# Optimization experiments

Hardware: AMD Instinct MI355X
Metric: run time of the kernel (lower is better)

The kernel has to match this reference:

```python
import jax, jax.numpy as jnp
import numpy as np

B, S, D = 2, 2048, 2048
H, KV, HD = 16, 4, 128          # n_heads, n_kv_heads, head_dim = d_model // n_heads
R = H // KV                      # n_rep (GQA group size)
THETA = 500000.0


def _rotate_half(x):
    x1, x2 = jnp.split(x, 2, axis=-1)
    return jnp.concatenate([-x2, x1], axis=-1)


def _rope_cos_sin(position_ids):
    # inv_freq over even dims, outer with positions, duplicated (LLaMA-style)
    inv_freq = 1.0 / (THETA ** (jnp.arange(0, HD, 2, dtype=jnp.float32) / HD))
    freqs = position_ids.astype(jnp.float32)[..., None] * inv_freq  # (B, S, HD/2)
    emb = jnp.concatenate([freqs, freqs], axis=-1)                  # (B, S, HD)
    return jnp.cos(emb)[:, None], jnp.sin(emb)[:, None]             # (B, 1, S, HD)


def setup_inputs() -> dict:
    key = jax.random.key(0)
    ks = jax.random.split(key, 5)
    x = jax.random.normal(ks[0], (B, S, D), dtype=jnp.float32)
    wq = jax.random.normal(ks[1], (D, H * HD), dtype=jnp.float32) * (D ** -0.5)
    wk = jax.random.normal(ks[2], (D, KV * HD), dtype=jnp.float32) * (D ** -0.5)
    wv = jax.random.normal(ks[3], (D, KV * HD), dtype=jnp.float32) * (D ** -0.5)
    wo = jax.random.normal(ks[4], (H * HD, D), dtype=jnp.float32) * (D ** -0.5)
    causal = jnp.tril(jnp.ones((S, S), dtype=bool))
    attn_mask = jnp.where(causal, 0.0, -1e9).astype(jnp.float32)[None, None]  # (1,1,S,S)
    position_ids = jnp.tile(jnp.arange(S, dtype=jnp.int32)[None, :], (B, 1))
    return {"x": x, "wq": wq, "wk": wk, "wv": wv, "wo": wo,
            "attn_mask": attn_mask, "position_ids": position_ids}


def reference(x, wq, wk, wv, wo, attn_mask, position_ids):
    b, s, _ = x.shape
    # projections (bias-free Linear) + head split, (B, heads, S, HD)
    q = (x @ wq).reshape(b, s, H, HD).transpose(0, 2, 1, 3)
    k = (x @ wk).reshape(b, s, KV, HD).transpose(0, 2, 1, 3)
    v = (x @ wv).reshape(b, s, KV, HD).transpose(0, 2, 1, 3)
    cos, sin = _rope_cos_sin(position_ids)
    q = q * cos + _rotate_half(q) * sin
    k = k * cos + _rotate_half(k) * sin
    # GQA: group q heads (B, KV, R, S, HD); equivalent to repeat_interleave on K/V
    qg = q.reshape(b, KV, R, s, HD)
    scores = jnp.einsum('bgrsd,bgtd->bgrst', qg.astype(jnp.float32),
                        k.astype(jnp.float32)) / np.float32(np.sqrt(HD))
    scores = scores + attn_mask[:, :, None]          # (1,1,1,S,S) broadcast
    p = jax.nn.softmax(scores, axis=-1).astype(x.dtype)
    out = jnp.einsum('bgrst,bgtd->bgrsd', p, v)      # (B, KV, R, S, HD)
    out = out.reshape(b, H, s, HD).transpose(0, 2, 1, 3).reshape(b, s, H * HD)
    return out @ wo
```

## Files before the change

kernel.cpp:

```cpp
#include <hip/hip_runtime.h>
#include <hip/hip_bf16.h>
#include <math.h>

#define Bsz 2
#define Sq  2048
#define Dm  2048
#define Hn  16
#define KVn 4
#define HDn 128

typedef __attribute__((ext_vector_type(8))) short bf16x8;
typedef __attribute__((ext_vector_type(4))) float f32x4;

__device__ __forceinline__ short f2b(float f) {
    __hip_bfloat16 h = __float2bfloat16(f);
    return *reinterpret_cast<short*>(&h);
}
__device__ __forceinline__ float b2f(short s) {
    __hip_bfloat16 h = *reinterpret_cast<__hip_bfloat16*>(&s);
    return __bfloat162float(h);
}

__global__ __launch_bounds__(256) void f2b_kernel(
    const float* __restrict__ X, short* __restrict__ Y, int n4)
{
    int i = blockIdx.x * 256 + threadIdx.x;
    if (i >= n4) return;
    float4 v = ((const float4*)X)[i];
    short4 o;
    o.x = f2b(v.x); o.y = f2b(v.y); o.z = f2b(v.z); o.w = f2b(v.w);
    ((short4*)Y)[i] = o;
}

__global__ __launch_bounds__(256) void wconv_all_kernel(
    const float* __restrict__ wq, const float* __restrict__ wk,
    const float* __restrict__ wv, const float* __restrict__ wo,
    short* __restrict__ wqkvT, short* __restrict__ woT)
{
    __shared__ float t[32][33];
    const int n0 = blockIdx.x * 32;
    const int k0 = blockIdx.y * 32;
    const int tx = threadIdx.x, ty = threadIdx.y;

    const float* W; int Nsec, nloc; short* dst;
    if (n0 < 2048)      { W = wq; Nsec = 2048; nloc = n0;        dst = wqkvT + (size_t)n0 * Dm; }
    else if (n0 < 2560) { W = wk; Nsec = 512;  nloc = n0 - 2048; dst = wqkvT + (size_t)n0 * Dm; }
    else if (n0 < 3072) { W = wv; Nsec = 512;  nloc = n0 - 2560; dst = wqkvT + (size_t)n0 * Dm; }
    else                { W = wo; Nsec = 2048; nloc = n0 - 3072; dst = woT + (size_t)(n0 - 3072) * Dm; }

#pragma unroll
    for (int r = 0; r < 4; ++r) {
        const int row = ty + 8 * r;
        t[row][tx] = W[(size_t)(k0 + row) * Nsec + nloc + tx];
    }
    __syncthreads();
#pragma unroll
    for (int r = 0; r < 4; ++r) {
        const int row = ty + 8 * r;
        dst[(size_t)row * Dm + k0 + tx] = f2b(t[tx][row]);
    }
}

template <typename OT>
__global__ __launch_bounds__(256) void gemm_bt_kernel(
    const short* __restrict__ A, const short* __restrict__ Bt,
    OT* __restrict__ C, int M, int N, int K)
{
    __shared__ __align__(16) short As[128 * 64];
    __shared__ __align__(16) short Bs[128 * 64];

    const int tid  = threadIdx.x;
    const int w    = tid >> 6;
    const int lane = tid & 63;
    const int m16  = lane & 15;
    const int g4   = lane >> 4;
    const int wm   = w >> 1, wn = w & 1;

    const int row0 = blockIdx.y * 128;
    const int col0 = blockIdx.x * 128;

    const short* Ab = A  + (size_t)row0 * K;
    const short* Bb = Bt + (size_t)col0 * K;

    const int trow = tid >> 3;
    const int soct = (tid & 7) ^ (trow & 7);

    f32x4 acc[4][4];
#pragma unroll
    for (int i = 0; i < 4; ++i)
#pragma unroll
        for (int j = 0; j < 4; ++j) acc[i][j] = (f32x4){0.f, 0.f, 0.f, 0.f};

    for (int k0 = 0; k0 < K; k0 += 64) {
#pragma unroll
        for (int r = 0; r < 4; ++r) {
            const short* gp = Ab + (size_t)(r * 32 + trow) * K + k0 + soct * 8;
            short* lp = &As[(size_t)(r * 256 + w * 64) * 8];
            __builtin_amdgcn_global_load_lds(
                (const __attribute__((address_space(1))) void*)gp,
                (__attribute__((address_space(3))) void*)lp, 16, 0, 0);
        }
#pragma unroll
        for (int r = 0; r < 4; ++r) {
            const short* gp = Bb + (size_t)(r * 32 + trow) * K + k0 + soct * 8;
            short* lp = &Bs[(size_t)(r * 256 + w * 64) * 8];
            __builtin_amdgcn_global_load_lds(
                (const __attribute__((address_space(1))) void*)gp,
                (__attribute__((address_space(3))) void*)lp, 16, 0, 0);
        }
        __syncthreads();

#pragma unroll
        for (int kc = 0; kc < 2; ++kc) {
            bf16x8 a[4], b[4];
            const int swz = (kc * 4 + g4) ^ (m16 & 7);
#pragma unroll
            for (int s = 0; s < 4; ++s) {
                const int rowA = wm * 64 + s * 16 + m16;
                a[s] = *(const bf16x8*)&As[rowA * 64 + swz * 8];
                const int rowB = wn * 64 + s * 16 + m16;
                b[s] = *(const bf16x8*)&Bs[rowB * 64 + swz * 8];
            }
#pragma unroll
            for (int i = 0; i < 4; ++i)
#pragma unroll
                for (int j = 0; j < 4; ++j)
                    acc[i][j] = __builtin_amdgcn_mfma_f32_16x16x32_bf16(
                        a[i], b[j], acc[i][j], 0, 0, 0);
        }
        __syncthreads();
    }

#pragma unroll
    for (int i = 0; i < 4; ++i) {
        const int mbase = row0 + wm * 64 + i * 16 + g4 * 4;
#pragma unroll
        for (int j = 0; j < 4; ++j) {
            const int n = col0 + wn * 64 + j * 16 + m16;
#pragma unroll
            for (int r = 0; r < 4; ++r) {
                if constexpr (sizeof(OT) == 2)
                    C[(size_t)(mbase + r) * N + n] = f2b(acc[i][j][r]);
                else
                    C[(size_t)(mbase + r) * N + n] = acc[i][j][r];
            }
        }
    }
}

__global__ __launch_bounds__(256) void rope_all_kernel(
    const short* __restrict__ C3b, short* __restrict__ Qb, short* __restrict__ Kb,
    const int* __restrict__ pos_ids, float qscale, int total)
{
    int idx = blockIdx.x * blockDim.x + threadIdx.x;
    if (idx >= total) return;
    const int i = idx & 63;
    int rest = idx >> 6;
    const int s = rest % Sq;
    const int b = rest / Sq;

    const int pos = pos_ids[b * Sq + s];
    const float e   = -(float)(2 * i) * (1.0f / (float)HDn);
    const float inv = exp2f(e * 18.931568569324174f);
    const float f   = (float)pos * inv;
    float sn, c;
    sincosf(f, &sn, &c);

    const short* src = C3b + ((size_t)(b * Sq + s)) * 3072;

#pragma unroll
    for (int h = 0; h < Hn; ++h) {
        const float x1 = b2f(src[h * HDn + i]);
        const float x2 = b2f(src[h * HDn + i + 64]);
        const size_t dst = (((size_t)b * Hn + h) * Sq + s) * HDn;
        Qb[dst + i]      = f2b((x1 * c - x2 * sn) * qscale);
        Qb[dst + i + 64] = f2b((x2 * c + x1 * sn) * qscale);
    }
#pragma unroll
    for (int h = 0; h < KVn; ++h) {
        const float x1 = b2f(src[2048 + h * HDn + i]);
        const float x2 = b2f(src[2048 + h * HDn + i + 64]);
        const size_t dst = (((size_t)b * KVn + h) * Sq + s) * HDn;
        Kb[dst + i]      = f2b(x1 * c - x2 * sn);
        Kb[dst + i + 64] = f2b(x2 * c + x1 * sn);
    }
}

__global__ __launch_bounds__(256) void vconv_kernel(
    const short* __restrict__ C3b, short* __restrict__ Vt)
{
    __shared__ short t[32][34];
    const int bk = blockIdx.z;
    const int b  = bk >> 2, kv = bk & 3;
    const int s0 = blockIdx.x * 32;
    const int d0 = blockIdx.y * 32;
    const int tx = threadIdx.x, ty = threadIdx.y;

#pragma unroll
    for (int r = 0; r < 4; ++r) {
        const int row = ty + 8 * r;
        t[row][tx] = C3b[((size_t)(b * Sq + s0 + row)) * 3072 + 2560 + kv * HDn + d0 + tx];
    }
    __syncthreads();
#pragma unroll
    for (int r = 0; r < 4; ++r) {
        const int row = ty + 8 * r;
        Vt[((size_t)bk * HDn + d0 + row) * Sq + s0 + tx] = t[tx][row];
    }
}

__global__ __launch_bounds__(256, 2) void fattn_kernel(
    const short* __restrict__ Qb, const short* __restrict__ Kb,
    const short* __restrict__ Vtb, short* __restrict__ AOb)
{
    __shared__ __align__(16) short Ks[2][64 * 128];
    __shared__ __align__(16) short Vs[2][128 * 64];

    const int tid  = threadIdx.x;
    const int w    = tid >> 6;
    const int lane = tid & 63;
    const int m16  = lane & 15;
    const int g4   = lane >> 4;

    const int i    = blockIdx.x;
    const int half = i >> 8;
    const int k4   = i & 15;
    const int p    = half ? k4 : 15 - k4;
    const int h    = (i >> 4) & 15;
    const int b    = i >> 8;
    const int kv   = h >> 2;

    const int htA = 31 - p, htB = p;
    const int nch = htA + 1;
    const int qA  = htA * 64 + w * 16;
    const int qB  = htB * 64 + w * 16;

    bf16x8 qfA[4], qfB[4];
    {
        const short* qpA = Qb + (((size_t)b * Hn + h) * Sq + qA + m16) * HDn + g4 * 8;
        const short* qpB = Qb + (((size_t)b * Hn + h) * Sq + qB + m16) * HDn + g4 * 8;
#pragma unroll
        for (int c = 0; c < 4; ++c) {
            qfA[c] = *(const bf16x8*)(qpA + c * 32);
            qfB[c] = *(const bf16x8*)(qpB + c * 32);
        }
    }

    const short* kbase = Kb  + ((size_t)b * KVn + kv) * Sq * HDn;
    const short* vbase = Vtb + ((size_t)b * KVn + kv) * (size_t)HDn * Sq;

    const short* gpK[4];
    const short* gpV[4];
#pragma unroll
    for (int r = 0; r < 4; ++r) {
        const int ci = r * 256 + tid;
        const int R  = ci >> 4, o = ci & 15;
        const int hf = (R >> 5) & 1, Rl = R & 31;
        const int phys = hf * 32 + ((Rl >> 2) & 3) * 8 + ((Rl >> 4) & 1) * 4 + (Rl & 3);
        gpK[r] = kbase + (size_t)phys * HDn + (o ^ (R & 7)) * 8;
        const int d = ci >> 3, ov = ci & 7;
        gpV[r] = vbase + (size_t)d * Sq + (ov ^ (d & 7)) * 8;
    }

    auto stage = [&](int ktE, int buf) {
#pragma unroll
        for (int r = 0; r < 4; ++r) {
            const short* gp = gpK[r] + (size_t)ktE * HDn;
            short* lp = &Ks[buf][(size_t)(r * 256 + w * 64) * 8];
            __builtin_amdgcn_global_load_lds(
                (const __attribute__((address_space(1))) void*)gp,
                (__attribute__((address_space(3))) void*)lp, 16, 0, 0);
        }
#pragma unroll
        for (int r = 0; r < 4; ++r) {
            const short* gp = gpV[r] + ktE;
            short* lp = &Vs[buf][(size_t)(r * 256 + w * 64) * 8];
            __builtin_amdgcn_global_load_lds(
                (const __attribute__((address_space(1))) void*)gp,
                (__attribute__((address_space(3))) void*)lp, 16, 0, 0);
        }
    };

    f32x4 OtA[8], OtB[8];
#pragma unroll
    for (int t = 0; t < 8; ++t) {
        OtA[t] = (f32x4){0.f, 0.f, 0.f, 0.f};
        OtB[t] = (f32x4){0.f, 0.f, 0.f, 0.f};
    }
    float mA = -1e30f, lA = 0.f, mB = -1e30f, lB = 0.f;

    stage(0, 0);
    int gpar = 0;

    for (int ch = 0; ch <= p; ++ch) {
        const int cur = gpar & 1; gpar ^= 1;
        const int kt  = ch << 6;

        __syncthreads();
        stage((ch + 1) << 6, cur ^ 1);

        const bool dgB = (ch == p);
        const short* KsC = Ks[cur];
        const short* VsC = Vs[cur];

        f32x4 sc0[4], sc1[4];
        __builtin_amdgcn_s_setprio(1);
#pragma unroll
        for (int f = 0; f < 4; ++f) {
            f32x4 a0 = (f32x4){0.f, 0.f, 0.f, 0.f};
            f32x4 a1 = (f32x4){0.f, 0.f, 0.f, 0.f};
            const int krow = f * 16 + m16;
#pragma unroll
            for (int c = 0; c < 4; ++c) {
                bf16x8 kf = *(const bf16x8*)&KsC[krow * 128 + (((c * 4 + g4) ^ (m16 & 7)) * 8)];
                a0 = __builtin_amdgcn_mfma_f32_16x16x32_bf16(kf, qfA[c], a0, 0, 0, 0);
                a1 = __builtin_amdgcn_mfma_f32_16x16x32_bf16(kf, qfB[c], a1, 0, 0, 0);
            }
            sc0[f] = a0; sc1[f] = a1;
        }
        __builtin_amdgcn_s_setprio(0);

        if (dgB) {
            const int qg = qB + m16;
#pragma unroll
            for (int f = 0; f < 4; ++f)
#pragma unroll
                for (int ii = 0; ii < 4; ++ii) {
                    const int kg = kt + (f >> 1) * 32 + g4 * 8 + (f & 1) * 4 + ii;
                    if (kg > qg) sc1[f][ii] = -1e30f;
                }
        }

        bf16x8 pf0[2], pf1[2];
        {
            float mx = sc0[0][0];
#pragma unroll
            for (int f = 0; f < 4; ++f)
#pragma unroll
                for (int ii = 0; ii < 4; ++ii) mx = fmaxf(mx, sc0[f][ii]);
            mx = fmaxf(mx, __shfl_xor(mx, 16));
            mx = fmaxf(mx, __shfl_xor(mx, 32));
            if (!__all(mx <= mA + 8.0f)) {
                const float nm = fmaxf(mA, mx);
                const float alpha = exp2f(mA - nm);
                mA = nm; lA *= alpha;
#pragma unroll
                for (int t = 0; t < 8; ++t)
#pragma unroll
                    for (int ii = 0; ii < 4; ++ii) OtA[t][ii] *= alpha;
            }
            float ps = 0.f;
#pragma unroll
            for (int f = 0; f < 4; ++f)
#pragma unroll
                for (int ii = 0; ii < 4; ++ii) {
                    sc0[f][ii] = exp2f(sc0[f][ii] - mA);
                    ps += sc0[f][ii];
                }
            ps += __shfl_xor(ps, 16);
            ps += __shfl_xor(ps, 32);
            lA += ps;
#pragma unroll
            for (int hf = 0; hf < 2; ++hf) {
                bf16x8 pk;
#pragma unroll
                for (int j8 = 0; j8 < 8; ++j8)
                    pk[j8] = f2b(j8 < 4 ? sc0[hf * 2][j8] : sc0[hf * 2 + 1][j8 - 4]);
                pf0[hf] = pk;
            }
        }
        {
            float mx = sc1[0][0];
#pragma unroll
            for (int f = 0; f < 4; ++f)
#pragma unroll
                for (int ii = 0; ii < 4; ++ii) mx = fmaxf(mx, sc1[f][ii]);
            mx = fmaxf(mx, __shfl_xor(mx, 16));
            mx = fmaxf(mx, __shfl_xor(mx, 32));
            if (!__all(mx <= mB + 8.0f)) {
                const float nm = fmaxf(mB, mx);
                const float alpha = exp2f(mB - nm);
                mB = nm; lB *= alpha;
#pragma unroll
                for (int t = 0; t < 8; ++t)
#pragma unroll
                    for (int ii = 0; ii < 4; ++ii) OtB[t][ii] *= alpha;
            }
            float ps = 0.f;
#pragma unroll
            for (int f = 0; f < 4; ++f)
#pragma unroll
                for (int ii = 0; ii < 4; ++ii) {
                    sc1[f][ii] = exp2f(sc1[f][ii] - mB);
                    ps += sc1[f][ii];
                }
            ps += __shfl_xor(ps, 16);
            ps += __shfl_xor(ps, 32);
            lB += ps;
#pragma unroll
            for (int hf = 0; hf < 2; ++hf) {
                bf16x8 pk;
#pragma unroll
                for (int j8 = 0; j8 < 8; ++j8)
                    pk[j8] = f2b(j8 < 4 ? sc1[hf * 2][j8] : sc1[hf * 2 + 1][j8 - 4]);
                pf1[hf] = pk;
            }
        }

        __builtin_amdgcn_s_setprio(1);
#pragma unroll
        for (int t = 0; t < 8; ++t) {
            const int d = t * 16 + m16;
            bf16x8 vfa = *(const bf16x8*)&VsC[d * 64 + ((g4 ^ (d & 7)) * 8)];
            bf16x8 vfb = *(const bf16x8*)&VsC[d * 64 + (((4 + g4) ^ (d & 7)) * 8)];
            OtA[t] = __builtin_amdgcn_mfma_f32_16x16x32_bf16(vfa, pf0[0], OtA[t], 0, 0, 0);
            OtA[t] = __builtin_amdgcn_mfma_f32_16x16x32_bf16(vfb, pf0[1], OtA[t], 0, 0, 0);
            OtB[t] = __builtin_amdgcn_mfma_f32_16x16x32_bf16(vfa, pf1[0], OtB[t], 0, 0, 0);
            OtB[t] = __builtin_amdgcn_mfma_f32_16x16x32_bf16(vfb, pf1[1], OtB[t], 0, 0, 0);
        }
        __builtin_amdgcn_s_setprio(0);
    }

    {
        const float inv = 1.0f / lB;
        short* op = AOb + ((size_t)(b * Sq + qB + m16)) * (Hn * HDn) + h * HDn + g4 * 4;
#pragma unroll
        for (int t = 0; t < 8; ++t) {
            short4 o;
            o.x = f2b(OtB[t][0] * inv);
            o.y = f2b(OtB[t][1] * inv);
            o.z = f2b(OtB[t][2] * inv);
            o.w = f2b(OtB[t][3] * inv);
            *(short4*)(op + t * 16) = o;
        }
    }

    for (int ch = p + 1; ch < nch; ++ch) {
        const int cur = gpar & 1; gpar ^= 1;
        const int kt  = ch << 6;

        __syncthreads();
        if (ch + 1 < nch) stage((ch + 1) << 6, cur ^ 1);

        const bool dgA = (ch == nch - 1);
        const short* KsC = Ks[cur];
        const short* VsC = Vs[cur];

        f32x4 sc[4];
        __builtin_amdgcn_s_setprio(1);
#pragma unroll
        for (int f = 0; f < 4; ++f) {
            f32x4 a = (f32x4){0.f, 0.f, 0.f, 0.f};
            const int krow = f * 16 + m16;
#pragma unroll
            for (int c = 0; c < 4; ++c) {
                bf16x8 kf = *(const bf16x8*)&KsC[krow * 128 + (((c * 4 + g4) ^ (m16 & 7)) * 8)];
                a = __builtin_amdgcn_mfma_f32_16x16x32_bf16(kf, qfA[c], a, 0, 0, 0);
            }
            sc[f] = a;
        }
        __builtin_amdgcn_s_setprio(0);

        if (dgA) {
            const int qg = qA + m16;
#pragma unroll
            for (int f = 0; f < 4; ++f)
#pragma unroll
                for (int ii = 0; ii < 4; ++ii) {
                    const int kg = kt + (f >> 1) * 32 + g4 * 8 + (f & 1) * 4 + ii;
                    if (kg > qg) sc[f][ii] = -1e30f;
                }
        }

        float mx = sc[0][0];
#pragma unroll
        for (int f = 0; f < 4; ++f)
#pragma unroll
            for (int ii = 0; ii < 4; ++ii) mx = fmaxf(mx, sc[f][ii]);
        mx = fmaxf(mx, __shfl_xor(mx, 16));
        mx = fmaxf(mx, __shfl_xor(mx, 32));
        if (!__all(mx <= mA + 8.0f)) {
            const float nm = fmaxf(mA, mx);
            const float alpha = exp2f(mA - nm);
            mA = nm; lA *= alpha;
#pragma unroll
            for (int t = 0; t < 8; ++t)
#pragma unroll
                for (int ii = 0; ii < 4; ++ii) OtA[t][ii] *= alpha;
        }
        float ps = 0.f;
#pragma unroll
        for (int f = 0; f < 4; ++f)
#pragma unroll
            for (int ii = 0; ii < 4; ++ii) {
                sc[f][ii] = exp2f(sc[f][ii] - mA);
                ps += sc[f][ii];
            }
        ps += __shfl_xor(ps, 16);
        ps += __shfl_xor(ps, 32);
        lA += ps;

        bf16x8 pf[2];
#pragma unroll
        for (int hf = 0; hf < 2; ++hf) {
            bf16x8 pk;
#pragma unroll
            for (int j8 = 0; j8 < 8; ++j8)
                pk[j8] = f2b(j8 < 4 ? sc[hf * 2][j8] : sc[hf * 2 + 1][j8 - 4]);
            pf[hf] = pk;
        }

        __builtin_amdgcn_s_setprio(1);
#pragma unroll
        for (int t = 0; t < 8; ++t) {
            const int d = t * 16 + m16;
            bf16x8 vfa = *(const bf16x8*)&VsC[d * 64 + ((g4 ^ (d & 7)) * 8)];
            bf16x8 vfb = *(const bf16x8*)&VsC[d * 64 + (((4 + g4) ^ (d & 7)) * 8)];
            OtA[t] = __builtin_amdgcn_mfma_f32_16x16x32_bf16(vfa, pf[0], OtA[t], 0, 0, 0);
            OtA[t] = __builtin_amdgcn_mfma_f32_16x16x32_bf16(vfb, pf[1], OtA[t], 0, 0, 0);
        }
        __builtin_amdgcn_s_setprio(0);
    }

    {
        const float inv = 1.0f / lA;
        short* op = AOb + ((size_t)(b * Sq + qA + m16)) * (Hn * HDn) + h * HDn + g4 * 4;
#pragma unroll
        for (int t = 0; t < 8; ++t) {
            short4 o;
            o.x = f2b(OtA[t][0] * inv);
            o.y = f2b(OtA[t][1] * inv);
            o.z = f2b(OtA[t][2] * inv);
            o.w = f2b(OtA[t][3] * inv);
            *(short4*)(op + t * 16) = o;
        }
    }
}

extern "C" void kernel_launch(void* const* d_in, const int* in_sizes, int n_in,
                              void* d_out, int out_size, void* d_ws, size_t ws_size,
                              hipStream_t stream)
{
    const float* x   = (const float*)d_in[0];
    const float* wq  = (const float*)d_in[1];
    const float* wk  = (const float*)d_in[2];
    const float* wv  = (const float*)d_in[3];
    const float* wo  = (const float*)d_in[4];
    const int* pos   = (const int*)d_in[6];
    float* out = (float*)d_out;

    const int M = Bsz * Sq;
    const size_t nX  = (size_t)M * Dm;

    short* xb    = (short*)d_ws;
    short* wqkvT = xb + nX;
    short* woT   = wqkvT + (size_t)3072 * Dm;
    short* C3b   = woT + (size_t)Dm * Dm;
    short* Qb    = C3b + (size_t)M * 3072;
    short* Kb    = Qb + nX;
    short* Vtb   = Kb + (size_t)Bsz * KVn * Sq * HDn;
    short* AOb   = Vtb + (size_t)Bsz * KVn * Sq * HDn;

    f2b_kernel<<<(nX / 4 + 255) / 256, 256, 0, stream>>>(x, xb, nX / 4);
    wconv_all_kernel<<<dim3(5120 / 32, Dm / 32), dim3(32, 8), 0, stream>>>(
        wq, wk, wv, wo, wqkvT, woT);

    gemm_bt_kernel<short><<<dim3(3072 / 128, M / 128), 256, 0, stream>>>(
        xb, wqkvT, C3b, M, 3072, Dm);

    {
        const float qscale = 0.08838834764831845f * 1.4426950408889634f;
        int tot = Bsz * Sq * 64;
        rope_all_kernel<<<(tot + 255) / 256, 256, 0, stream>>>(
            C3b, Qb, Kb, pos, qscale, tot);
    }
    vconv_kernel<<<dim3(Sq / 32, HDn / 32, Bsz * KVn), dim3(32, 8), 0, stream>>>(
        C3b, Vtb);

    fattn_kernel<<<Bsz * Hn * 16, 256, 0, stream>>>(Qb, Kb, Vtb, AOb);

    gemm_bt_kernel<float><<<dim3(Dm / 128, M / 128), 256, 0, stream>>>(
        AOb, woT, out, M, Dm, Dm);
}
```

Baseline: 315.4 us.

## Merge prep and rope/V kernels, add XCD-aware block swizzle to GEMM

Combines the x conversion and weight transpose kernels into one launch, and the RoPE and V-transpose kernels into another, each branching on block index. This cuts the launch count and lets independent work overlap inside a single grid. The GEMM also remaps its linear block index so that consecutive blocks land on the same XCD, aiming to improve L2 reuse on MI355X. The branching kernels share one shared-memory declaration, and the swizzle assumes the block count divides evenly by 8.

```diff
diff --git a/kernel.cpp b/kernel.cpp
--- a/kernel.cpp
+++ b/kernel.cpp
@@ -21,26 +21,31 @@
     return __bfloat162float(h);
 }
 
-__global__ __launch_bounds__(256) void f2b_kernel(
-    const float* __restrict__ X, short* __restrict__ Y, int n4)
-{
-    int i = blockIdx.x * 256 + threadIdx.x;
-    if (i >= n4) return;
-    float4 v = ((const float4*)X)[i];
-    short4 o;
-    o.x = f2b(v.x); o.y = f2b(v.y); o.z = f2b(v.z); o.w = f2b(v.w);
-    ((short4*)Y)[i] = o;
-}
-
-__global__ __launch_bounds__(256) void wconv_all_kernel(
+#define NB_F2B 8192
+#define NB_WC  10240
+__global__ __launch_bounds__(256) void prep_kernel(
+    const float* __restrict__ X, short* __restrict__ Y,
     const float* __restrict__ wq, const float* __restrict__ wk,
     const float* __restrict__ wv, const float* __restrict__ wo,
     short* __restrict__ wqkvT, short* __restrict__ woT)
 {
     __shared__ float t[32][33];
-    const int n0 = blockIdx.x * 32;
-    const int k0 = blockIdx.y * 32;
-    const int tx = threadIdx.x, ty = threadIdx.y;
+    const int bid = blockIdx.x;
+    const int tid = threadIdx.x;
+
+    if (bid < NB_F2B) {
+        const int i = bid * 256 + tid;
+        float4 v = ((const float4*)X)[i];
+        short4 o;
+        o.x = f2b(v.x); o.y = f2b(v.y); o.z = f2b(v.z); o.w = f2b(v.w);
+        ((short4*)Y)[i] = o;
+        return;
+    }
+
+    const int wb = bid - NB_F2B;
+    const int n0 = (wb % 160) * 32;
+    const int k0 = (wb / 160) * 32;
+    const int tx = tid & 31, ty = tid >> 5;
 
     const float* W; int Nsec, nloc; short* dst;
     if (n0 < 2048)      { W = wq; Nsec = 2048; nloc = n0;        dst = wqkvT + (size_t)n0 * Dm; }
@@ -76,8 +81,15 @@
     const int g4   = lane >> 4;
     const int wm   = w >> 1, wn = w & 1;
 
-    const int row0 = blockIdx.y * 128;
-    const int col0 = blockIdx.x * 128;
+    const int nwg = gridDim.x * gridDim.y;
+    const int lin = blockIdx.y * gridDim.x + blockIdx.x;
+    const int qq  = nwg >> 3;
+    const int sw  = (lin & 7) * qq + (lin >> 3);
+    const int bx  = sw % gridDim.x;
+    const int by  = sw / gridDim.x;
+
+    const int row0 = by * 128;
+    const int col0 = bx * 128;
 
     const short* Ab = A  + (size_t)row0 * K;
     const short* Bb = Bt + (size_t)col0 * K;
@@ -148,64 +160,71 @@
     }
 }
 
-__global__ __launch_bounds__(256) void rope_all_kernel(
+#define NB_ROPE 1024
+#define NB_VC   2048
+__global__ __launch_bounds__(256) void rv_kernel(
     const short* __restrict__ C3b, short* __restrict__ Qb, short* __restrict__ Kb,
-    const int* __restrict__ pos_ids, float qscale, int total)
+    short* __restrict__ Vt, const int* __restrict__ pos_ids, float qscale)
 {
-    int idx = blockIdx.x * blockDim.x + threadIdx.x;
-    if (idx >= total) return;
-    const int i = idx & 63;
-    int rest = idx >> 6;
-    const int s = rest % Sq;
-    const int b = rest / Sq;
-
-    const int pos = pos_ids[b * Sq + s];
-    const float e   = -(float)(2 * i) * (1.0f / (float)HDn);
-    const float inv = exp2f(e * 18.931568569324174f);
-    const float f   = (float)pos * inv;
-    float sn, c;
-    sincosf(f, &sn, &c);
-
-    const short* src = C3b + ((size_t)(b * Sq + s)) * 3072;
-
-#pragma unroll
-    for (int h = 0; h < Hn; ++h) {
-        const float x1 = b2f(src[h * HDn + i]);
-        const float x2 = b2f(src[h * HDn + i + 64]);
-        const size_t dst = (((size_t)b * Hn + h) * Sq + s) * HDn;
-        Qb[dst + i]      = f2b((x1 * c - x2 * sn) * qscale);
-        Qb[dst + i + 64] = f2b((x2 * c + x1 * sn) * qscale);
-    }
-#pragma unroll
-    for (int h = 0; h < KVn; ++h) {
-        const float x1 = b2f(src[2048 + h * HDn + i]);
-        const float x2 = b2f(src[2048 + h * HDn + i + 64]);
-        const size_t dst = (((size_t)b * KVn + h) * Sq + s) * HDn;
-        Kb[dst + i]      = f2b(x1 * c - x2 * sn);
-        Kb[dst + i + 64] = f2b(x2 * c + x1 * sn);
-    }
-}
-
-__global__ __launch_bounds__(256) void vconv_kernel(
-    const short* __restrict__ C3b, short* __restrict__ Vt)
-{
-    __shared__ short t[32][34];
-    const int bk = blockIdx.z;
+    __shared__ short tv[32][34];
+    const int bid = blockIdx.x;
+    const int tid = threadIdx.x;
+
+    if (bid < NB_ROPE) {
+        const int idx = bid * 256 + tid;
+        const int i = idx & 63;
+        int rest = idx >> 6;
+        const int s = rest % Sq;
+        const int b = rest / Sq;
+
+        const int pos = pos_ids[b * Sq + s];
+        const float e   = -(float)(2 * i) * (1.0f / (float)HDn);
+        const float inv = exp2f(e * 18.931568569324174f);
+        const float f   = (float)pos * inv;
+        float sn, c;
+        sincosf(f, &sn, &c);
+
+        const short* src = C3b + ((size_t)(b * Sq + s)) * 3072;
+
+#pragma unroll
+        for (int h = 0; h < Hn; ++h) {
+            const float x1 = b2f(src[h * HDn + i]);
+            const float x2 = b2f(src[h * HDn + i + 64]);
+            const size_t dst = (((size_t)b * Hn + h) * Sq + s) * HDn;
+            Qb[dst + i]      = f2b((x1 * c - x2 * sn) * qscale);
+            Qb[dst + i + 64] = f2b((x2 * c + x1 * sn) * qscale);
+        }
+#pragma unroll
+        for (int h = 0; h < KVn; ++h) {
+            const float x1 = b2f(src[2048 + h * HDn + i]);
+            const float x2 = b2f(src[2048 + h * HDn + i + 64]);
+            const size_t dst = (((size_t)b * KVn + h) * Sq + s) * HDn;
+            Kb[dst + i]      = f2b(x1 * c - x2 * sn);
+            Kb[dst + i + 64] = f2b(x2 * c + x1 * sn);
+        }
+        return;
+    }
+
+    const int lin = bid - NB_ROPE;
+    const int bxv = lin & 63;
+    const int rest = lin >> 6;
+    const int byv = rest & 3;
+    const int bk  = rest >> 2;
     const int b  = bk >> 2, kv = bk & 3;
-    const int s0 = blockIdx.x * 32;
-    const int d0 = blockIdx.y * 32;
-    const int tx = threadIdx.x, ty = threadIdx.y;
+    const int s0 = bxv * 32;
+    const int d0 = byv * 32;
+    const int tx = tid & 31, ty = tid >> 5;
 
 #pragma unroll
     for (int r = 0; r < 4; ++r) {
         const int row = ty + 8 * r;
-        t[row][tx] = C3b[((size_t)(b * Sq + s0 + row)) * 3072 + 2560 + kv * HDn + d0 + tx];
+        tv[row][tx] = C3b[((size_t)(b * Sq + s0 + row)) * 3072 + 2560 + kv * HDn + d0 + tx];
     }
     __syncthreads();
 #pragma unroll
     for (int r = 0; r < 4; ++r) {
         const int row = ty + 8 * r;
-        Vt[((size_t)bk * HDn + d0 + row) * Sq + s0 + tx] = t[tx][row];
+        Vt[((size_t)bk * HDn + d0 + row) * Sq + s0 + tx] = tv[tx][row];
     }
 }
 
@@ -561,21 +580,17 @@
     short* Vtb   = Kb + (size_t)Bsz * KVn * Sq * HDn;
     short* AOb   = Vtb + (size_t)Bsz * KVn * Sq * HDn;
 
-    f2b_kernel<<<(nX / 4 + 255) / 256, 256, 0, stream>>>(x, xb, nX / 4);
-    wconv_all_kernel<<<dim3(5120 / 32, Dm / 32), dim3(32, 8), 0, stream>>>(
-        wq, wk, wv, wo, wqkvT, woT);
+    prep_kernel<<<NB_F2B + NB_WC, 256, 0, stream>>>(
+        x, xb, wq, wk, wv, wo, wqkvT, woT);
 
     gemm_bt_kernel<short><<<dim3(3072 / 128, M / 128), 256, 0, stream>>>(
         xb, wqkvT, C3b, M, 3072, Dm);
 
     {
         const float qscale = 0.08838834764831845f * 1.4426950408889634f;
-        int tot = Bsz * Sq * 64;
-        rope_all_kernel<<<(tot + 255) / 256, 256, 0, stream>>>(
-            C3b, Qb, Kb, pos, qscale, tot);
-    }
-    vconv_kernel<<<dim3(Sq / 32, HDn / 32, Bsz * KVn), dim3(32, 8), 0, stream>>>(
-        C3b, Vtb);
+        rv_kernel<<<NB_ROPE + NB_VC, 256, 0, stream>>>(
+            C3b, Qb, Kb, Vtb, pos, qscale);
+    }
 
     fattn_kernel<<<Bsz * Hn * 16, 256, 0, stream>>>(Qb, Kb, Vtb, AOb);
 
```

Result: no change. 317.3 us (+0.6%).
